# Kernel optimization log

Measured on AMD Instinct MI355X. Metric: run time of the kernel, lower is better.

## Reference

```python
import math
import jax, jax.numpy as jnp
import numpy as np

B, S, E = 2, 2048, 2048
H, D = 16, 128

def setup_inputs() -> dict:
    key = jax.random.key(0)
    ks = jax.random.split(key, 5)
    scale = 0.02
    return {
        "hidden_states": jax.random.normal(ks[0], (B, S, E), dtype=jnp.float32),
        "Wq": jax.random.normal(ks[1], (E, E), dtype=jnp.float32) * scale,
        "Wk": jax.random.normal(ks[2], (E, E), dtype=jnp.float32) * scale,
        "Wv": jax.random.normal(ks[3], (E, E), dtype=jnp.float32) * scale,
        "Wo": jax.random.normal(ks[4], (E, E), dtype=jnp.float32) * scale,
        "bo": jnp.zeros((E,), dtype=jnp.float32),
    }

def _split_heads(x):
    # [B,S,E] -> [B,H,S,D]
    b, s, _ = x.shape
    return x.reshape(b, s, H, D).transpose(0, 2, 1, 3)

def reference(hidden_states, Wq, Wk, Wv, Wo, bo):
    # torch nn.Linear: y = x @ W.T (q/k/v have no bias)
    q = _split_heads(hidden_states @ Wq.T)
    k = _split_heads(hidden_states @ Wk.T)
    v = _split_heads(hidden_states @ Wv.T)
    scores = jnp.einsum("bhqd,bhkd->bhqk", q, k) / math.sqrt(D)
    # causal mask: strictly-upper-triangular positions set to -inf ...
    causal = jnp.triu(jnp.ones((S, S), dtype=bool), k=1)
    scores = jnp.where(causal[None, None], -jnp.inf, scores)
    # ... then clamped to [-1e4, 1e4] (so masked logits become -10000, not -inf)
    scores = jnp.clip(scores, -10000.0, 10000.0)
    attn = jax.nn.softmax(scores, axis=-1)
    out = jnp.einsum("bhqk,bhkd->bhqd", attn, v)  # [B,H,S,D]
    out = out.transpose(0, 2, 1, 3).reshape(B, S, E)  # merge heads
    return out @ Wo.T + bo
```

## Files before the change

kernel.cpp:

```cpp
#include <hip/hip_runtime.h>
#include <hip/hip_bf16.h>
#include <stdint.h>
#include <math.h>

#define B_ 2
#define S_ 2048
#define E_ 2048
#define H_ 16
#define D_ 128
#define M_ (B_*S_)

#define QSCALE 0.1275174308f

typedef _Float16 half8 __attribute__((ext_vector_type(8)));
typedef _Float16 half4 __attribute__((ext_vector_type(4)));
typedef float    floatx4 __attribute__((ext_vector_type(4)));

__device__ __forceinline__ void async_copy16(const void* g, void* lds_base) {
    __builtin_amdgcn_global_load_lds(
        (__attribute__((address_space(1))) void*)(uintptr_t)g,
        (__attribute__((address_space(3))) void*)(uint32_t)(uintptr_t)lds_base,
        16, 0, 0);
}

template<int CTRL>
__device__ __forceinline__ float dpp_mv(float x) {
    return __int_as_float(__builtin_amdgcn_update_dpp(
        0, __float_as_int(x), CTRL, 0xF, 0xF, true));
}
__device__ __forceinline__ float row_max16(float x) {
    x = fmaxf(x, dpp_mv<0xB1>(x));
    x = fmaxf(x, dpp_mv<0x4E>(x));
    x = fmaxf(x, dpp_mv<0x124>(x));
    x = fmaxf(x, dpp_mv<0x128>(x));
    return x;
}
__device__ __forceinline__ float row_sum16(float x) {
    x += dpp_mv<0xB1>(x);
    x += dpp_mv<0x4E>(x);
    x += dpp_mv<0x124>(x);
    x += dpp_mv<0x128>(x);
    return x;
}
__device__ __forceinline__ float fexp2(float x) {
    float r; __asm__("v_exp_f32 %0, %1" : "=v"(r) : "v"(x)); return r;
}

__global__ __launch_bounds__(256) void cast_all(
    const float* __restrict__ X,  const float* __restrict__ Wq,
    const float* __restrict__ Wk, const float* __restrict__ Wv,
    const float* __restrict__ Wo,
    _Float16* __restrict__ Xh,  _Float16* __restrict__ Wqh,
    _Float16* __restrict__ Wkh, _Float16* __restrict__ Wvh,
    _Float16* __restrict__ Woh)
{
    const int z = blockIdx.z;
    const float* in; _Float16* out; size_t off = 0;
    switch (z) {
        case 0: in = X;  out = Xh;  off = 0;        break;
        case 1: in = X;  out = Xh;  off = 1048576;  break;
        case 2: in = Wq; out = Wqh; break;
        case 3: in = Wk; out = Wkh; break;
        case 4: in = Wv; out = Wvh; break;
        default: in = Wo; out = Woh; break;
    }
    size_t i = off + (size_t)blockIdx.x * 256 + threadIdx.x;
    floatx4 v = ((const floatx4*)in)[i];
    ((half4*)out)[i] = __builtin_convertvector(v, half4);
}

#define GBUF (128*64 + 256*64)

__device__ __forceinline__ void stage512(
    const _Float16* __restrict__ gsrc, int ldk,
    _Float16* lbase, int slot0, int wave, int lane)
{
    int slot = slot0 + wave*64 + lane;
    int row  = slot >> 3;
    int sg   = (slot & 7) ^ (row & 7);
    async_copy16(gsrc + (size_t)row * ldk + sg * 8,
                 lbase + (slot0 + wave*64) * 8);
}

template<bool BIAS, typename OutT, int NW, bool TRV>
__global__ __launch_bounds__(512, 2) void gemm_bt(
    const _Float16* __restrict__ A,
    const _Float16* __restrict__ W0, const _Float16* __restrict__ W1,
    const _Float16* __restrict__ W2,
    OutT* __restrict__ C0, OutT* __restrict__ C1, OutT* __restrict__ C2,
    const float* __restrict__ bias, int M, int N, int K)
{
    const _Float16* W = W0; OutT* C = C0;
    if (NW > 1) {
        if (blockIdx.y == 1) { W = W1; C = C1; }
        else if (blockIdx.y == 2) { W = W2; C = C2; }
    }
    __shared__ __align__(16) _Float16 sm[3 * GBUF];

    const int tid  = threadIdx.x;
    const int lane = tid & 63;
    const int wave = tid >> 6;
    const int wm = wave >> 2, wn = wave & 3;
    const int fr = lane & 15, fg = lane >> 4;

    const int bx = blockIdx.x;
    const int n_tile = bx & 7;
    const int m_tile = bx >> 3;
    const int m0 = m_tile * 128;
    const int n0 = n_tile * 256;

    const int NT = K >> 6;

#pragma unroll
    for (int pt = 0; pt < 2; ++pt) {
        _Float16* ab = &sm[pt * GBUF];
        _Float16* bb = ab + 128*64;
        const _Float16* Ag = A + (size_t)m0 * K + pt*64;
        const _Float16* Wg = W + (size_t)n0 * K + pt*64;
        stage512(Ag, K, ab, 0,    wave, lane);
        stage512(Ag, K, ab, 512,  wave, lane);
        stage512(Wg, K, bb, 0,    wave, lane);
        stage512(Wg, K, bb, 512,  wave, lane);
        stage512(Wg, K, bb, 1024, wave, lane);
        stage512(Wg, K, bb, 1536, wave, lane);
    }

    floatx4 acc[4][4] = {};

    for (int t = 0; t < NT; ++t) {
        if (t + 1 < NT) { __asm__ __volatile__("s_waitcnt vmcnt(6)" ::: "memory"); }
        else            { __asm__ __volatile__("s_waitcnt vmcnt(0)" ::: "memory"); }
        __builtin_amdgcn_sched_barrier(0);
        __builtin_amdgcn_s_barrier();
        __builtin_amdgcn_sched_barrier(0);

        const _Float16* Ab = &sm[(t % 3) * GBUF];
        const _Float16* Bb = Ab + 128*64;
        const bool pf = (t + 2 < NT);
        _Float16* pab = &sm[((t + 2) % 3) * GBUF];
        _Float16* pbb = pab + 128*64;
        const _Float16* pAg = A + (size_t)m0 * K + (t + 2)*64;
        const _Float16* pWg = W + (size_t)n0 * K + (t + 2)*64;

        half8 af[4][2], bf[4][2];
#pragma unroll
        for (int mt = 0; mt < 4; ++mt)
#pragma unroll
            for (int kk = 0; kk < 2; ++kk) {
                int row = wm*64 + mt*16 + fr;
                int g = (kk*4 + fg) ^ (row & 7);
                af[mt][kk] = *(const half8*)&Ab[row*64 + g*8];
            }
#pragma unroll
        for (int nt = 0; nt < 4; ++nt)
#pragma unroll
            for (int kk = 0; kk < 2; ++kk) {
                int row = wn*64 + nt*16 + fr;
                int g = (kk*4 + fg) ^ (row & 7);
                bf[nt][kk] = *(const half8*)&Bb[row*64 + g*8];
            }

        if (pf) {
            stage512(pAg, K, pab, 0,    wave, lane);
            stage512(pAg, K, pab, 512,  wave, lane);
            stage512(pWg, K, pbb, 0,    wave, lane);
            stage512(pWg, K, pbb, 512,  wave, lane);
            stage512(pWg, K, pbb, 1024, wave, lane);
            stage512(pWg, K, pbb, 1536, wave, lane);
        }

        __builtin_amdgcn_s_setprio(1);
#pragma unroll
        for (int kk = 0; kk < 2; ++kk)
#pragma unroll
            for (int nt = 0; nt < 4; ++nt)
#pragma unroll
                for (int mt = 0; mt < 4; ++mt)
                    acc[mt][nt] = __builtin_amdgcn_mfma_f32_16x16x32_f16(
                        af[mt][kk], bf[nt][kk], acc[mt][nt], 0, 0, 0);
        __builtin_amdgcn_s_setprio(0);
    }

    if (TRV && NW > 1 && blockIdx.y == 2) {
        _Float16* Vt = (_Float16*)C;
#pragma unroll
        for (int mt = 0; mt < 4; ++mt)
#pragma unroll
            for (int nt = 0; nt < 4; ++nt) {
                int col  = n0 + wn*64 + nt*16 + fr;
                int row0 = m0 + wm*64 + mt*16 + fg*4;
                int bq = row0 >> 11, s0 = row0 & 2047;
                int hq = col >> 7,  dq = col & 127;
                half4 v;
#pragma unroll
                for (int r = 0; r < 4; ++r) v[r] = (_Float16)acc[mt][nt][r];
                *(half4*)&Vt[(((size_t)(bq*16 + hq) * 128 + dq) << 11) + s0] = v;
            }
    } else {
        const float qs = (NW > 1 && blockIdx.y == 0) ? QSCALE : 1.f;
#pragma unroll
        for (int mt = 0; mt < 4; ++mt)
#pragma unroll
            for (int nt = 0; nt < 4; ++nt) {
                int col = n0 + wn*64 + nt*16 + fr;
                float bv = BIAS ? bias[col] : 0.f;
#pragma unroll
                for (int r = 0; r < 4; ++r) {
                    int row = m0 + wm*64 + mt*16 + fg*4 + r;
                    C[(size_t)row * N + col] = (OutT)(acc[mt][nt][r] * qs + bv);
                }
            }
    }
}

__global__ __launch_bounds__(256, 2) void attn_causal_coop(
    const _Float16* __restrict__ Q, const _Float16* __restrict__ K,
    const _Float16* __restrict__ Vt, _Float16* __restrict__ O)
{
    const int n   = blockIdx.x;
    const int xcd = n & 7;
    const int idx = n >> 3;
    const int bh  = xcd * 4 + (idx >> 4);
    const int j   = idx & 15;
    const int b = bh >> 4, h = bh & 15;
    const int tid = threadIdx.x, lane = tid & 63, wave = tid >> 6;
    const int fr = lane & 15, fg = lane >> 4;

    __shared__ __align__(16) _Float16 Ks[64*128];
    __shared__ __align__(16) _Float16 Vs[128*64];
    __shared__ __align__(16) _Float16 Ps[4][32*72];

    const int rhi = (31 - j) * 64 + wave * 16;
    const int rlo = j * 64 + wave * 16;
    const int nkt = 32 - j;

    half8 qf[2][4];
    {
        const _Float16* qb0 = Q + ((size_t)(b*S_) + rhi) * E_ + h*D_;
        const _Float16* qb1 = Q + ((size_t)(b*S_) + rlo) * E_ + h*D_;
#pragma unroll
        for (int kk = 0; kk < 4; ++kk) {
            qf[0][kk] = *(const half8*)&qb0[(size_t)fr * E_ + kk*32 + fg*8];
            qf[1][kk] = *(const half8*)&qb1[(size_t)fr * E_ + kk*32 + fg*8];
        }
    }

    float m_i[2][4], l_i[2][4];
    floatx4 o[2][8] = {};
#pragma unroll
    for (int mt = 0; mt < 2; ++mt)
#pragma unroll
        for (int r = 0; r < 4; ++r) { m_i[mt][r] = -INFINITY; l_i[mt][r] = 0.f; }

    const _Float16* kg = K + (size_t)(b*S_) * E_ + h*D_;
    const _Float16* vg = Vt + (size_t)bh * D_ * S_;
    _Float16* ps = &Ps[wave][0];

    for (int jt = 0; jt < nkt; ++jt) {
        __syncthreads();
#pragma unroll
        for (int q = 0; q < 4; ++q) {
            int G = q*256 + tid;
            int row = G >> 4, slot = G & 15;
            int c = slot ^ (row & 7);
            async_copy16(kg + (size_t)(jt*64 + row) * E_ + c*8,
                         &Ks[(q*256 + wave*64) * 8]);
        }
#pragma unroll
        for (int q = 0; q < 4; ++q) {
            int G = q*256 + tid;
            int row = G >> 3, slot = G & 7;
            int c = slot ^ (row & 7);
            async_copy16(vg + (size_t)row * S_ + jt*64 + c*8,
                         &Vs[(q*256 + wave*64) * 8]);
        }
        __syncthreads();

        const bool lo_act = (jt <= j);

        floatx4 sacc[2][4] = {};
#pragma unroll
        for (int kk = 0; kk < 4; ++kk) {
            half8 bf[4];
#pragma unroll
            for (int nt = 0; nt < 4; ++nt)
                bf[nt] = *(const half8*)
                    &Ks[(nt*16 + fr)*128 + (((kk*4 + fg) ^ (fr & 7)) * 8)];
#pragma unroll
            for (int nt = 0; nt < 4; ++nt)
                sacc[0][nt] = __builtin_amdgcn_mfma_f32_16x16x32_f16(
                    qf[0][kk], bf[nt], sacc[0][nt], 0, 0, 0);
            if (lo_act) {
#pragma unroll
                for (int nt = 0; nt < 4; ++nt)
                    sacc[1][nt] = __builtin_amdgcn_mfma_f32_16x16x32_f16(
                        qf[1][kk], bf[nt], sacc[1][nt], 0, 0, 0);
            }
        }

        const int kc0 = jt*64 + fr;
#pragma unroll
        for (int mt = 0; mt < 2; ++mt) {
            if (mt == 1 && !lo_act) continue;
            const bool diag = mt ? (jt == j) : (jt == nkt - 1);
            const int qr0 = (mt ? rlo : rhi) + fg*4;
            float alpha[4];
#pragma unroll
            for (int r = 0; r < 4; ++r) {
                float mx;
                if (diag) {
                    mx = -INFINITY;
#pragma unroll
                    for (int nt = 0; nt < 4; ++nt) {
                        float s = sacc[mt][nt][r];
                        s = (kc0 + nt*16 <= qr0 + r) ? s : -INFINITY;
                        sacc[mt][nt][r] = s;
                        mx = fmaxf(mx, s);
                    }
                } else {
                    mx = fmaxf(fmaxf(sacc[mt][0][r], sacc[mt][1][r]),
                               fmaxf(sacc[mt][2][r], sacc[mt][3][r]));
                }
                mx = row_max16(mx);
                float mnew = fmaxf(m_i[mt][r], mx);
                alpha[r] = (m_i[mt][r] == -INFINITY) ? 0.f : fexp2(m_i[mt][r] - mnew);
                float rs = 0.f;
#pragma unroll
                for (int nt = 0; nt < 4; ++nt) {
                    float p = fexp2(sacc[mt][nt][r] - mnew);
                    sacc[mt][nt][r] = p;
                    rs += p;
                }
                rs = row_sum16(rs);
                l_i[mt][r] = alpha[r] * l_i[mt][r] + rs;
                m_i[mt][r] = mnew;
            }
#pragma unroll
            for (int dt = 0; dt < 8; ++dt)
#pragma unroll
                for (int r = 0; r < 4; ++r) o[mt][dt][r] *= alpha[r];

#pragma unroll
            for (int nt = 0; nt < 4; ++nt)
#pragma unroll
                for (int r = 0; r < 4; ++r)
                    ps[(mt*16 + fg*4 + r)*72 + nt*16 + fr] = (_Float16)sacc[mt][nt][r];
        }
        __asm__ __volatile__("s_waitcnt lgkmcnt(0)" ::: "memory");
        __builtin_amdgcn_sched_barrier(0);

#pragma unroll
        for (int kk = 0; kk < 2; ++kk) {
            half8 pf0 = *(const half8*)&ps[(fr)*72 + kk*32 + fg*8];
            half8 pf1 = *(const half8*)&ps[(16 + fr)*72 + kk*32 + fg*8];
#pragma unroll
            for (int dt = 0; dt < 8; ++dt) {
                half8 vf = *(const half8*)
                    &Vs[(dt*16 + fr)*64 + (((kk*4 + fg) ^ (fr & 7)) * 8)];
                o[0][dt] = __builtin_amdgcn_mfma_f32_16x16x32_f16(
                    pf0, vf, o[0][dt], 0, 0, 0);
                if (lo_act)
                    o[1][dt] = __builtin_amdgcn_mfma_f32_16x16x32_f16(
                        pf1, vf, o[1][dt], 0, 0, 0);
            }
        }
    }

#pragma unroll
    for (int mt = 0; mt < 2; ++mt) {
        const int rbase = mt ? rlo : rhi;
        _Float16* ob = O + ((size_t)(b*S_) + rbase) * E_ + h*D_;
#pragma unroll
        for (int r = 0; r < 4; ++r) {
            float inv = 1.f / l_i[mt][r];
#pragma unroll
            for (int dt = 0; dt < 8; ++dt)
                ob[(size_t)(fg*4 + r) * E_ + dt*16 + fr] = (_Float16)(o[mt][dt][r] * inv);
        }
    }
}

extern "C" void kernel_launch(void* const* d_in, const int* in_sizes, int n_in,
                              void* d_out, int out_size, void* d_ws, size_t ws_size,
                              hipStream_t stream) {
    const float* X  = (const float*)d_in[0];
    const float* Wq = (const float*)d_in[1];
    const float* Wk = (const float*)d_in[2];
    const float* Wv = (const float*)d_in[3];
    const float* Wo = (const float*)d_in[4];
    const float* bo = (const float*)d_in[5];
    float* out = (float*)d_out;

    const size_t ME = (size_t)M_ * E_;
    const size_t EE = (size_t)E_ * E_;
    _Float16* ws  = (_Float16*)d_ws;
    _Float16* Xh  = ws;
    _Float16* Wqh = Xh  + ME;
    _Float16* Wkh = Wqh + EE;
    _Float16* Wvh = Wkh + EE;
    _Float16* Woh = Wvh + EE;
    _Float16* Qh  = Woh + EE;
    _Float16* Kh  = Qh  + ME;
    _Float16* Vth = Kh  + ME;
    _Float16* Oh  = Xh;

    cast_all<<<dim3(4096, 1, 6), dim3(256), 0, stream>>>(
        X, Wq, Wk, Wv, Wo, Xh, Wqh, Wkh, Wvh, Woh);

    gemm_bt<false, _Float16, 3, true><<<dim3(256, 3), dim3(512), 0, stream>>>(
        Xh, Wqh, Wkh, Wvh, Qh, Kh, Vth, nullptr, M_, E_, E_);

    attn_causal_coop<<<dim3(512), dim3(256), 0, stream>>>(Qh, Kh, Vth, Oh);

    gemm_bt<true, float, 1, false><<<dim3(256, 1), dim3(512), 0, stream>>>(
        Oh, Woh, nullptr, nullptr, out, nullptr, nullptr, bo, M_, E_, E_);
}
```

Baseline: 381.1 us.

## Shrink GEMM tiles to 128x128 with 4 waves and double buffering

Changes the projection GEMMs from 128x256 tiles with 8 waves and a 3-stage LDS ring to 128x128 tiles with 4 waves and a 2-stage ring. Twice as many blocks are launched, and each block uses less LDS, which could allow more blocks per CU and better load balance across CUs. The trade-off is a shallower prefetch: the loop now waits for all outstanding loads every iteration, and the smaller tiles reuse each loaded operand less, raising global and LDS traffic per FLOP.

```diff
diff --git a/kernel.cpp b/kernel.cpp
--- a/kernel.cpp
+++ b/kernel.cpp
@@ -69,7 +69,7 @@
     ((half4*)out)[i] = __builtin_convertvector(v, half4);
 }
 
-#define GBUF (128*64 + 256*64)
+#define GBUF (128*64 + 128*64)
 
 __device__ __forceinline__ void stage512(
     const _Float16* __restrict__ gsrc, int ldk,
@@ -83,7 +83,7 @@
 }
 
 template<bool BIAS, typename OutT, int NW, bool TRV>
-__global__ __launch_bounds__(512, 2) void gemm_bt(
+__global__ __launch_bounds__(256, 2) void gemm_bt(
     const _Float16* __restrict__ A,
     const _Float16* __restrict__ W0, const _Float16* __restrict__ W1,
     const _Float16* __restrict__ W2,
@@ -95,52 +95,56 @@
         if (blockIdx.y == 1) { W = W1; C = C1; }
         else if (blockIdx.y == 2) { W = W2; C = C2; }
     }
-    __shared__ __align__(16) _Float16 sm[3 * GBUF];
+    __shared__ __align__(16) _Float16 sm[2 * GBUF];
 
     const int tid  = threadIdx.x;
     const int lane = tid & 63;
     const int wave = tid >> 6;
-    const int wm = wave >> 2, wn = wave & 3;
+    const int wm = wave >> 1, wn = wave & 1;
     const int fr = lane & 15, fg = lane >> 4;
 
     const int bx = blockIdx.x;
-    const int n_tile = bx & 7;
-    const int m_tile = bx >> 3;
+    const int n_tile = bx & 15;
+    const int m_tile = bx >> 4;
     const int m0 = m_tile * 128;
-    const int n0 = n_tile * 256;
+    const int n0 = n_tile * 128;
 
     const int NT = K >> 6;
 
-#pragma unroll
-    for (int pt = 0; pt < 2; ++pt) {
-        _Float16* ab = &sm[pt * GBUF];
+    {
+        _Float16* ab = &sm[0];
         _Float16* bb = ab + 128*64;
-        const _Float16* Ag = A + (size_t)m0 * K + pt*64;
-        const _Float16* Wg = W + (size_t)n0 * K + pt*64;
-        stage512(Ag, K, ab, 0,    wave, lane);
-        stage512(Ag, K, ab, 512,  wave, lane);
-        stage512(Wg, K, bb, 0,    wave, lane);
-        stage512(Wg, K, bb, 512,  wave, lane);
-        stage512(Wg, K, bb, 1024, wave, lane);
-        stage512(Wg, K, bb, 1536, wave, lane);
+        const _Float16* Ag = A + (size_t)m0 * K;
+        const _Float16* Wg = W + (size_t)n0 * K;
+#pragma unroll
+        for (int s0 = 0; s0 < 1024; s0 += 256) {
+            stage512(Ag, K, ab, s0, wave, lane);
+            stage512(Wg, K, bb, s0, wave, lane);
+        }
     }
 
     floatx4 acc[4][4] = {};
 
     for (int t = 0; t < NT; ++t) {
-        if (t + 1 < NT) { __asm__ __volatile__("s_waitcnt vmcnt(6)" ::: "memory"); }
-        else            { __asm__ __volatile__("s_waitcnt vmcnt(0)" ::: "memory"); }
+        __asm__ __volatile__("s_waitcnt vmcnt(0)" ::: "memory");
         __builtin_amdgcn_sched_barrier(0);
         __builtin_amdgcn_s_barrier();
         __builtin_amdgcn_sched_barrier(0);
 
-        const _Float16* Ab = &sm[(t % 3) * GBUF];
+        const _Float16* Ab = &sm[(t & 1) * GBUF];
         const _Float16* Bb = Ab + 128*64;
-        const bool pf = (t + 2 < NT);
-        _Float16* pab = &sm[((t + 2) % 3) * GBUF];
-        _Float16* pbb = pab + 128*64;
-        const _Float16* pAg = A + (size_t)m0 * K + (t + 2)*64;
-        const _Float16* pWg = W + (size_t)n0 * K + (t + 2)*64;
+
+        if (t + 1 < NT) {
+            _Float16* pab = &sm[((t + 1) & 1) * GBUF];
+            _Float16* pbb = pab + 128*64;
+            const _Float16* pAg = A + (size_t)m0 * K + (t + 1)*64;
+            const _Float16* pWg = W + (size_t)n0 * K + (t + 1)*64;
+#pragma unroll
+            for (int s0 = 0; s0 < 1024; s0 += 256) {
+                stage512(pAg, K, pab, s0, wave, lane);
+                stage512(pWg, K, pbb, s0, wave, lane);
+            }
+        }
 
         half8 af[4][2], bf[4][2];
 #pragma unroll
@@ -159,15 +163,6 @@
                 int g = (kk*4 + fg) ^ (row & 7);
                 bf[nt][kk] = *(const half8*)&Bb[row*64 + g*8];
             }
-
-        if (pf) {
-            stage512(pAg, K, pab, 0,    wave, lane);
-            stage512(pAg, K, pab, 512,  wave, lane);
-            stage512(pWg, K, pbb, 0,    wave, lane);
-            stage512(pWg, K, pbb, 512,  wave, lane);
-            stage512(pWg, K, pbb, 1024, wave, lane);
-            stage512(pWg, K, pbb, 1536, wave, lane);
-        }
 
         __builtin_amdgcn_s_setprio(1);
 #pragma unroll
@@ -407,11 +402,11 @@
     cast_all<<<dim3(4096, 1, 6), dim3(256), 0, stream>>>(
         X, Wq, Wk, Wv, Wo, Xh, Wqh, Wkh, Wvh, Woh);
 
-    gemm_bt<false, _Float16, 3, true><<<dim3(256, 3), dim3(512), 0, stream>>>(
+    gemm_bt<false, _Float16, 3, true><<<dim3(512, 3), dim3(256), 0, stream>>>(
         Xh, Wqh, Wkh, Wvh, Qh, Kh, Vth, nullptr, M_, E_, E_);
 
     attn_causal_coop<<<dim3(512), dim3(256), 0, stream>>>(Qh, Kh, Vth, Oh);
 
-    gemm_bt<true, float, 1, false><<<dim3(256, 1), dim3(512), 0, stream>>>(
+    gemm_bt<true, float, 1, false><<<dim3(512, 1), dim3(256), 0, stream>>>(
         Oh, Woh, nullptr, nullptr, out, nullptr, nullptr, bo, M_, E_, E_);
 }
```

After: 368.1 us. 3.4% less time.
